# Optimization experiments

Measured on AMD Instinct MI355X. Metric: run time of the kernel, lower is better.

The kernel has to match this reference:

```python
import jax, jax.numpy as jnp
import numpy as np

IN_DIM = 512
CMP_DIM = 512
OUT_DIM = 512
BOARD = (8, 8, 8, 8)
BATCH = 4


def setup_inputs() -> dict:
    key = jax.random.key(0)
    ks = jax.random.split(key, 9)
    shape = (BATCH,) + BOARD + (IN_DIM,)
    query_X = jax.random.normal(ks[0], shape, dtype=jnp.float32)
    key_X = jax.random.normal(ks[1], shape, dtype=jnp.float32)
    value_X = jax.random.normal(ks[2], shape, dtype=jnp.float32)
    s = 1.0 / np.sqrt(IN_DIM)
    W_Q = jax.random.uniform(ks[3], (IN_DIM, CMP_DIM), jnp.float32, -s, s)
    b_Q = jax.random.uniform(ks[4], (CMP_DIM,), jnp.float32, -s, s)
    W_K = jax.random.uniform(ks[5], (IN_DIM, CMP_DIM), jnp.float32, -s, s)
    b_K = jax.random.uniform(ks[6], (CMP_DIM,), jnp.float32, -s, s)
    W_V = jax.random.uniform(ks[7], (IN_DIM, OUT_DIM), jnp.float32, -s, s)
    b_V = jax.random.uniform(ks[8], (OUT_DIM,), jnp.float32, -s, s)
    return {"query_X": query_X, "key_X": key_X, "value_X": value_X,
            "W_Q": W_Q, "b_Q": b_Q, "W_K": W_K, "b_K": b_K, "W_V": W_V, "b_V": b_V}


def reference(query_X, key_X, value_X, W_Q, b_Q, W_K, b_K, W_V, b_V):
    B = query_X.shape[0]
    # project then flatten board dims: (B, N, d)
    q = (query_X @ W_Q + b_Q).reshape(B, -1, CMP_DIM)
    k = (key_X @ W_K + b_K).reshape(B, -1, CMP_DIM)
    v = (value_X @ W_V + b_V).reshape(B, -1, OUT_DIM)
    scores = jnp.einsum('bqc,bkc->bqk', q, k) / jnp.sqrt(jnp.float32(CMP_DIM))
    att = jax.nn.softmax(scores, axis=-1)
    return jnp.einsum('bqk,bkd->bqd', att, v)
```

## Files before the change

### kernel.cpp

```cpp
#include <hip/hip_runtime.h>
#include <hip/hip_bf16.h>
#include <stdint.h>


typedef __attribute__((ext_vector_type(8))) short short8;
typedef __attribute__((ext_vector_type(4))) short short4v;
typedef __attribute__((ext_vector_type(4))) float f32x4;

#define SCALE_L2E 0.06375880243f
#define FIXED_M   12.0f

__device__ __forceinline__ short f2bf(float f) {
    union { float f; uint32_t u; } v; v.f = f;
    uint32_t r = (v.u + 0x7fffu + ((v.u >> 16) & 1u)) >> 16;
    return (short)r;
}

__device__ __forceinline__ f32x4 mfma16x16x32(short8 a, short8 b, f32x4 c) {
    return __builtin_amdgcn_mfma_f32_16x16x32_bf16(a, b, c, 0, 0, 0);
}

#define GLOAD_LDS16(gp, lp)                                                      \
    __builtin_amdgcn_global_load_lds(                                            \
        (const __attribute__((address_space(1))) uint32_t*)(gp),                 \
        (__attribute__((address_space(3))) uint32_t*)(lp), 16, 0, 0)

__global__ __launch_bounds__(256) void cvt_all(
        const float* __restrict__ qX, const float* __restrict__ kX,
        const float* __restrict__ vX,
        const float* __restrict__ WQ, const float* __restrict__ WK,
        const float* __restrict__ WV,
        short* __restrict__ xq, short* __restrict__ xk, short* __restrict__ xv,
        short* __restrict__ wqt, short* __restrict__ wkt, short* __restrict__ wvt) {
    __shared__ float tile[32][33];
    const int y = blockIdx.y;
    if (y < 3) {
        const float* x = y == 0 ? qX : (y == 1 ? kX : vX);
        short*       o = y == 0 ? xq : (y == 1 ? xk : xv);
        int i = blockIdx.x * 256 + threadIdx.x;
        float4 v = ((const float4*)x)[i];
        short4v s;
        s.x = f2bf(v.x); s.y = f2bf(v.y); s.z = f2bf(v.z); s.w = f2bf(v.w);
        ((short4v*)o)[i] = s;
    } else {
        if (blockIdx.x >= 768) return;
        int wz = blockIdx.x >> 8;
        int rem = blockIdx.x & 255;
        int bx = rem & 15, by = rem >> 4;
        const float* src = wz == 0 ? WQ : (wz == 1 ? WK : WV);
        short*       dst = wz == 0 ? wqt : (wz == 1 ? wkt : wvt);
        int tx = threadIdx.x & 31, ty = threadIdx.x >> 5;
        int n0 = bx * 32, k0 = by * 32;
#pragma unroll
        for (int j = 0; j < 32; j += 8)
            tile[ty + j][tx] = src[(size_t)(k0 + ty + j) * 512 + n0 + tx];
        __syncthreads();
#pragma unroll
        for (int j = 0; j < 32; j += 8)
            dst[(size_t)(n0 + ty + j) * 512 + k0 + tx] = f2bf(tile[tx][ty + j]);
    }
}

__device__ __forceinline__ void proj_body(
        const short* __restrict__ Xb, const short* __restrict__ WT,
        const float* __restrict__ bias, short* __restrict__ out, int transpose_v,
        short* sA, short* sB, short* sT) {
    const int tid = threadIdx.x;
    const int w = tid >> 6, lane = tid & 63;
    const int l15 = lane & 15, quad = lane >> 4;
    const int wr = w >> 1, wc = w & 1;
    const int m0 = blockIdx.x * 128;
    const int n0 = blockIdx.y * 128;

    f32x4 acc[4][4];
#pragma unroll
    for (int i = 0; i < 4; ++i)
#pragma unroll
        for (int j = 0; j < 4; ++j) acc[i][j] = f32x4{0.f, 0.f, 0.f, 0.f};

    for (int k0 = 0; k0 < 512; k0 += 64) {
        __syncthreads();
#pragma unroll
        for (int p = 0; p < 4; ++p) {
            int i = p * 256 + tid;
            int row = i >> 3, cl = i & 7, cg = cl ^ (row & 7);
            GLOAD_LDS16(Xb + (size_t)(m0 + row) * 512 + k0 + cg * 8,
                        sA + (size_t)(i & ~63) * 8);
        }
#pragma unroll
        for (int p = 0; p < 4; ++p) {
            int i = p * 256 + tid;
            int row = i >> 3, cl = i & 7, cg = cl ^ (row & 7);
            GLOAD_LDS16(WT + (size_t)(n0 + row) * 512 + k0 + cg * 8,
                        sB + (size_t)(i & ~63) * 8);
        }
        __syncthreads();
#pragma unroll
        for (int ks = 0; ks < 2; ++ks) {
            short8 af[4], bfr[4];
#pragma unroll
            for (int mt = 0; mt < 4; ++mt) {
                int row = wr * 64 + mt * 16 + l15;
                int c = (ks * 4 + quad) ^ (row & 7);
                af[mt] = *(const short8*)&sA[(row * 8 + c) * 8];
            }
#pragma unroll
            for (int nt = 0; nt < 4; ++nt) {
                int row = wc * 64 + nt * 16 + l15;
                int c = (ks * 4 + quad) ^ (row & 7);
                bfr[nt] = *(const short8*)&sB[(row * 8 + c) * 8];
            }
#pragma unroll
            for (int mt = 0; mt < 4; ++mt)
#pragma unroll
                for (int nt = 0; nt < 4; ++nt)
                    acc[mt][nt] = mfma16x16x32(af[mt], bfr[nt], acc[mt][nt]);
        }
    }
    if (!transpose_v) {
#pragma unroll
        for (int nt = 0; nt < 4; ++nt) {
            float bv = bias[n0 + wc * 64 + nt * 16 + l15];
#pragma unroll
            for (int mt = 0; mt < 4; ++mt)
#pragma unroll
                for (int r = 0; r < 4; ++r) {
                    int gm = m0 + wr * 64 + mt * 16 + quad * 4 + r;
                    int gn = n0 + wc * 64 + nt * 16 + l15;
                    out[(size_t)gm * 512 + gn] = f2bf(acc[mt][nt][r] + bv);
                }
        }
    } else {
        __syncthreads();
#pragma unroll
        for (int nt = 0; nt < 4; ++nt) {
            float bv = bias[n0 + wc * 64 + nt * 16 + l15];
            int dl = wc * 64 + nt * 16 + l15;
#pragma unroll
            for (int mt = 0; mt < 4; ++mt) {
                int pl = wr * 64 + mt * 16 + quad * 4;
                short4v s;
                s.x = f2bf(acc[mt][nt][0] + bv);
                s.y = f2bf(acc[mt][nt][1] + bv);
                s.z = f2bf(acc[mt][nt][2] + bv);
                s.w = f2bf(acc[mt][nt][3] + bv);
                *(short4v*)&sT[dl * 136 + pl] = s;
            }
        }
        __syncthreads();
        const int b = m0 >> 12, posb = m0 & 4095;
        const int col = (tid & 15) * 8;
#pragma unroll
        for (int rnd = 0; rnd < 8; ++rnd) {
            int dl = rnd * 16 + (tid >> 4);
            *(short8*)&out[((size_t)b * 512 + n0 + dl) * 4096 + posb + col] =
                *(const short8*)&sT[dl * 136 + col];
        }
    }
}

__global__ __launch_bounds__(256) void proj3(
        const short* __restrict__ xq, const short* __restrict__ xk,
        const short* __restrict__ xv,
        const short* __restrict__ wqt, const short* __restrict__ wkt,
        const short* __restrict__ wvt,
        const float* __restrict__ bQ, const float* __restrict__ bK,
        const float* __restrict__ bV,
        short* __restrict__ oq, short* __restrict__ ok, short* __restrict__ ovt) {
    __shared__ __align__(16) short smem[128 * 136];
    const int z = blockIdx.z;
    proj_body(z == 0 ? xq : (z == 1 ? xk : xv),
              z == 0 ? wqt : (z == 1 ? wkt : wvt),
              z == 0 ? bQ : (z == 1 ? bK : bV),
              z == 0 ? oq : (z == 1 ? ok : ovt), z == 2 ? 1 : 0,
              smem, smem + 8192, smem);
}

__global__ __launch_bounds__(256) void prep_wt(
        const float* __restrict__ wq, const float* __restrict__ wk,
        const float* __restrict__ wv,
        short* __restrict__ wqt, short* __restrict__ wkt, short* __restrict__ wvt) {
    __shared__ float tile[32][33];
    const float* src = blockIdx.z == 0 ? wq : (blockIdx.z == 1 ? wk : wv);
    short*       dst = blockIdx.z == 0 ? wqt : (blockIdx.z == 1 ? wkt : wvt);
    int tx = threadIdx.x, ty = threadIdx.y;
    int n0 = blockIdx.x * 32, k0 = blockIdx.y * 32;
#pragma unroll
    for (int j = 0; j < 32; j += 8)
        tile[ty + j][tx] = src[(size_t)(k0 + ty + j) * 512 + n0 + tx];
    __syncthreads();
#pragma unroll
    for (int j = 0; j < 32; j += 8)
        dst[(size_t)(n0 + ty + j) * 512 + k0 + tx] = f2bf(tile[tx][ty + j]);
}

__global__ __launch_bounds__(256) void x2bf(
        const float* __restrict__ x, short* __restrict__ y) {
    int i = blockIdx.x * 256 + threadIdx.x;
    float4 v = ((const float4*)x)[i];
    short4v s;
    s.x = f2bf(v.x); s.y = f2bf(v.y); s.z = f2bf(v.z); s.w = f2bf(v.w);
    ((short4v*)y)[i] = s;
}

__global__ __launch_bounds__(256) void proj_gemm2(
        const short* __restrict__ Xb, const short* __restrict__ WT,
        const float* __restrict__ bias, short* __restrict__ out, int transpose_v) {
    __shared__ __align__(16) short smem[128 * 136];
    proj_body(Xb, WT, bias, out, transpose_v, smem, smem + 8192, smem);
}

__global__ __launch_bounds__(512, 2) void flash_attn(
        const short* __restrict__ qb, const short* __restrict__ kb,
        const short* __restrict__ vtb, float* __restrict__ out) {
    __shared__ __align__(16) short sK[64 * 64 * 8];
    __shared__ __align__(16) short sV[512 * 8 * 8];
    __shared__ __align__(16) short sP[64 * 72];
    __shared__ __align__(16) float sL[64 * 4];

    const int tid = threadIdx.x;
    const int w = tid >> 6, lane = tid & 63;
    const int l15 = lane & 15, quad = lane >> 4;
    const int qg = w >> 2, kg = w & 3;

    const int n = blockIdx.x + (blockIdx.y << 6);
    const int batch = (n >> 1) & 3;
    const int q0 = ((((n >> 3) << 1) | (n & 1))) << 6;

    const short* qbase = qb  + (size_t)batch * 4096 * 512;
    const short* kbase = kb  + (size_t)batch * 4096 * 512;
    const short* vbase = vtb + (size_t)batch * 512 * 4096;

    const int key0 = tid >> 6;
    const int kcg  = (tid & 63) ^ (key0 & 7);
    const short* ksrc0 = kbase + (size_t)key0 * 512 + kcg * 8;
    const int kdst0 = (tid & ~63) * 8;
    const int d0  = tid >> 3;
    const int vcg = (tid & 7) ^ (d0 & 7);
    const short* vsrc0 = vbase + (size_t)d0 * 4096 + vcg * 8;
    const int vdst0 = (tid & ~63) * 8;

    short8 qf[2][16];
#pragma unroll
    for (int qmt = 0; qmt < 2; ++qmt) {
        const short* qrow = qbase + (size_t)(q0 + qg * 32 + qmt * 16 + l15) * 512 + quad * 8;
#pragma unroll
        for (int ks = 0; ks < 16; ++ks)
            qf[qmt][ks] = *(const short8*)(qrow + ks * 32);
    }

    f32x4 acc[4][4];
#pragma unroll
    for (int i = 0; i < 4; ++i)
#pragma unroll
        for (int j = 0; j < 4; ++j) acc[i][j] = f32x4{0.f, 0.f, 0.f, 0.f};
    float lp[2][4] = {{0.f, 0.f, 0.f, 0.f}, {0.f, 0.f, 0.f, 0.f}};

#pragma unroll
    for (int it = 0; it < 8; ++it)
        GLOAD_LDS16(ksrc0 + it * 4096, sK + kdst0 + it * 4096);
    __syncthreads();

    for (int t = 0; t < 64; ++t) {
        const int t0 = t * 64;

        {
            const short* vp = vsrc0 + t0;
#pragma unroll
            for (int it = 0; it < 8; ++it)
                GLOAD_LDS16(vp + (size_t)it * 262144, sV + vdst0 + it * 4096);
        }
        __builtin_amdgcn_sched_barrier(0);

        f32x4 s0 = f32x4{0.f, 0.f, 0.f, 0.f};
        f32x4 s1 = f32x4{0.f, 0.f, 0.f, 0.f};
        const int key = kg * 16 + l15;
        const int ksw = key & 7;
        __builtin_amdgcn_s_setprio(1);
#pragma unroll
        for (int ks = 0; ks < 16; ++ks) {
            short8 kf = *(const short8*)&sK[(key * 64 + ((ks * 4 + quad) ^ ksw)) * 8];
            s0 = mfma16x16x32(qf[0][ks], kf, s0);
            s1 = mfma16x16x32(qf[1][ks], kf, s1);
        }
        __builtin_amdgcn_s_setprio(0);
#pragma unroll
        for (int qmt = 0; qmt < 2; ++qmt) {
            f32x4 sv = qmt ? s1 : s0;
#pragma unroll
            for (int r = 0; r < 4; ++r) {
                float p = __builtin_amdgcn_exp2f(
                    __builtin_fmaf(sv[r], SCALE_L2E, -FIXED_M));
                lp[qmt][r] += p;
                sP[(qg * 32 + qmt * 16 + quad * 4 + r) * 72 + kg * 16 + l15] = f2bf(p);
            }
        }

        __syncthreads();

        if (t < 63) {
            const short* kp = ksrc0 + (size_t)(t0 + 64) * 512;
#pragma unroll
            for (int it = 0; it < 8; ++it)
                GLOAD_LDS16(kp + it * 4096, sK + kdst0 + it * 4096);
        }
        __builtin_amdgcn_sched_barrier(0);

        __builtin_amdgcn_s_setprio(1);
#pragma unroll
        for (int kc = 0; kc < 2; ++kc) {
            short8 pa[4], vf[4];
#pragma unroll
            for (int mt = 0; mt < 4; ++mt)
                pa[mt] = *(const short8*)&sP[(mt * 16 + l15) * 72 + kc * 32 + quad * 8];
#pragma unroll
            for (int nt = 0; nt < 4; ++nt) {
                int d = w * 64 + nt * 16 + l15;
                vf[nt] = *(const short8*)&sV[(d * 8 + ((kc * 4 + quad) ^ (d & 7))) * 8];
            }
#pragma unroll
            for (int mt = 0; mt < 4; ++mt)
#pragma unroll
                for (int nt = 0; nt < 4; ++nt)
                    acc[mt][nt] = mfma16x16x32(pa[mt], vf[nt], acc[mt][nt]);
        }
        __builtin_amdgcn_s_setprio(0);

        __syncthreads();
    }
#pragma unroll
    for (int qmt = 0; qmt < 2; ++qmt)
#pragma unroll
        for (int r = 0; r < 4; ++r) {
            float v = lp[qmt][r];
            v += __shfl_xor(v, 1);
            v += __shfl_xor(v, 2);
            v += __shfl_xor(v, 4);
            v += __shfl_xor(v, 8);
            if (l15 == 0)
                sL[(qg * 32 + qmt * 16 + quad * 4 + r) * 4 + kg] = v;
        }
    __syncthreads();
#pragma unroll
    for (int mt = 0; mt < 4; ++mt)
#pragma unroll
        for (int r = 0; r < 4; ++r) {
            int row = mt * 16 + quad * 4 + r;
            float linv = 1.0f / (sL[row * 4] + sL[row * 4 + 1] +
                                 sL[row * 4 + 2] + sL[row * 4 + 3]);
            float* orow = out + ((size_t)batch * 4096 + q0 + row) * 512 + w * 64 + l15;
#pragma unroll
            for (int nt = 0; nt < 4; ++nt)
                orow[nt * 16] = acc[mt][nt][r] * linv;
        }
}

extern "C" void kernel_launch(void* const* d_in, const int* in_sizes, int n_in,
                              void* d_out, int out_size, void* d_ws, size_t ws_size,
                              hipStream_t stream) {
    const float* qX = (const float*)d_in[0];
    const float* kX = (const float*)d_in[1];
    const float* vX = (const float*)d_in[2];
    const float* WQ = (const float*)d_in[3];
    const float* bQ = (const float*)d_in[4];
    const float* WK = (const float*)d_in[5];
    const float* bK = (const float*)d_in[6];
    const float* WV = (const float*)d_in[7];
    const float* bV = (const float*)d_in[8];
    float* out = (float*)d_out;

    short* qb  = (short*)d_ws;
    short* kb  = qb  + (size_t)16384 * 512;
    short* vtb = kb  + (size_t)16384 * 512;
    short* wqt = vtb + (size_t)16384 * 512;
    short* wkt = wqt + (size_t)512 * 512;
    short* wvt = wkt + (size_t)512 * 512;
    short* xq  = wvt + (size_t)512 * 512;

    if (ws_size >= (size_t)102236160) {
        short* xk = xq + (size_t)16384 * 512;
        short* xv = xk + (size_t)16384 * 512;
        cvt_all<<<dim3(8192, 4), 256, 0, stream>>>(qX, kX, vX, WQ, WK, WV,
                                                   xq, xk, xv, wqt, wkt, wvt);
        proj3<<<dim3(128, 4, 3), 256, 0, stream>>>(xq, xk, xv, wqt, wkt, wvt,
                                                   bQ, bK, bV, qb, kb, vtb);
    } else {
        prep_wt<<<dim3(16, 16, 3), dim3(32, 8), 0, stream>>>(WQ, WK, WV, wqt, wkt, wvt);
        x2bf<<<8192, 256, 0, stream>>>(qX, xq);
        proj_gemm2<<<dim3(128, 4), 256, 0, stream>>>(xq, wqt, bQ, qb, 0);
        x2bf<<<8192, 256, 0, stream>>>(kX, xq);
        proj_gemm2<<<dim3(128, 4), 256, 0, stream>>>(xq, wkt, bK, kb, 0);
        x2bf<<<8192, 256, 0, stream>>>(vX, xq);
        proj_gemm2<<<dim3(128, 4), 256, 0, stream>>>(xq, wvt, bV, vtb, 1);
    }
    flash_attn<<<dim3(64, 4), 512, 0, stream>>>(qb, kb, vtb, out);
}
```

Before: 359.1 us.

## Shrink flash-attention tiles to 32 queries x 32 keys with 256-thread blocks

Restructures the attention kernel from 64-query blocks of 512 threads with 64-key steps to 32-query blocks of 256 threads with 32-key steps, doubling the grid to 512 blocks. Each wave now owns 128 output columns and one 16-row score tile, and the K/V LDS layouts and swizzles are reworked to match. The s_setprio hints are removed. The aim is more blocks in flight across the CUs with a smaller LDS footprint, in exchange for reading K and V twice as often in total and running twice as many loop iterations and barriers.

```diff
diff --git a/kernel.cpp b/kernel.cpp
--- a/kernel.cpp
+++ b/kernel.cpp
@@ -210,147 +210,133 @@
     proj_body(Xb, WT, bias, out, transpose_v, smem, smem + 8192, smem);
 }
 
-__global__ __launch_bounds__(512, 2) void flash_attn(
+__global__ __launch_bounds__(256, 2) void flash_attn(
         const short* __restrict__ qb, const short* __restrict__ kb,
         const short* __restrict__ vtb, float* __restrict__ out) {
-    __shared__ __align__(16) short sK[64 * 64 * 8];
-    __shared__ __align__(16) short sV[512 * 8 * 8];
-    __shared__ __align__(16) short sP[64 * 72];
-    __shared__ __align__(16) float sL[64 * 4];
+    __shared__ __align__(16) short sK[32 * 512];
+    __shared__ __align__(16) short sV[512 * 32];
+    __shared__ __align__(16) short sP[32 * 56];
+    __shared__ __align__(16) float sL[32 * 2];
 
     const int tid = threadIdx.x;
     const int w = tid >> 6, lane = tid & 63;
     const int l15 = lane & 15, quad = lane >> 4;
-    const int qg = w >> 2, kg = w & 3;
-
-    const int n = blockIdx.x + (blockIdx.y << 6);
+    const int qg = w >> 1, kg = w & 1;
+
+    const int n = blockIdx.x + (blockIdx.y << 7);
     const int batch = (n >> 1) & 3;
-    const int q0 = ((((n >> 3) << 1) | (n & 1))) << 6;
+    const int q0 = ((((n >> 3) << 1) | (n & 1))) << 5;
 
     const short* qbase = qb  + (size_t)batch * 4096 * 512;
     const short* kbase = kb  + (size_t)batch * 4096 * 512;
     const short* vbase = vtb + (size_t)batch * 512 * 4096;
 
-    const int key0 = tid >> 6;
-    const int kcg  = (tid & 63) ^ (key0 & 7);
-    const short* ksrc0 = kbase + (size_t)key0 * 512 + kcg * 8;
+    const int ko0 = (lane ^ (w & 7)) * 8;
+    const int ko1 = (lane ^ ((w + 4) & 7)) * 8;
     const int kdst0 = (tid & ~63) * 8;
-    const int d0  = tid >> 3;
-    const int vcg = (tid & 7) ^ (d0 & 7);
-    const short* vsrc0 = vbase + (size_t)d0 * 4096 + vcg * 8;
+
+    const short* vsrc0 = vbase + (size_t)(tid >> 2) * 4096
+                       + (((tid & 3) ^ ((tid >> 3) & 3)) * 8);
     const int vdst0 = (tid & ~63) * 8;
 
-    short8 qf[2][16];
-#pragma unroll
-    for (int qmt = 0; qmt < 2; ++qmt) {
-        const short* qrow = qbase + (size_t)(q0 + qg * 32 + qmt * 16 + l15) * 512 + quad * 8;
+    short8 qf[16];
+    {
+        const short* qrow = qbase + (size_t)(q0 + qg * 16 + l15) * 512 + quad * 8;
 #pragma unroll
         for (int ks = 0; ks < 16; ++ks)
-            qf[qmt][ks] = *(const short8*)(qrow + ks * 32);
-    }
-
-    f32x4 acc[4][4];
-#pragma unroll
-    for (int i = 0; i < 4; ++i)
-#pragma unroll
-        for (int j = 0; j < 4; ++j) acc[i][j] = f32x4{0.f, 0.f, 0.f, 0.f};
-    float lp[2][4] = {{0.f, 0.f, 0.f, 0.f}, {0.f, 0.f, 0.f, 0.f}};
+            qf[ks] = *(const short8*)(qrow + ks * 32);
+    }
+
+    f32x4 acc[2][8];
+#pragma unroll
+    for (int i = 0; i < 2; ++i)
+#pragma unroll
+        for (int j = 0; j < 8; ++j) acc[i][j] = f32x4{0.f, 0.f, 0.f, 0.f};
+    float lp[4] = {0.f, 0.f, 0.f, 0.f};
 
 #pragma unroll
     for (int it = 0; it < 8; ++it)
-        GLOAD_LDS16(ksrc0 + it * 4096, sK + kdst0 + it * 4096);
+        GLOAD_LDS16(kbase + (size_t)(it * 4 + w) * 512 + ((it & 1) ? ko1 : ko0),
+                    sK + it * 2048 + kdst0);
     __syncthreads();
 
-    for (int t = 0; t < 64; ++t) {
-        const int t0 = t * 64;
+    for (int t = 0; t < 128; ++t) {
+        const int t0 = t * 32;
 
         {
             const short* vp = vsrc0 + t0;
 #pragma unroll
             for (int it = 0; it < 8; ++it)
-                GLOAD_LDS16(vp + (size_t)it * 262144, sV + vdst0 + it * 4096);
+                GLOAD_LDS16(vp + (size_t)it * 262144, sV + it * 2048 + vdst0);
         }
         __builtin_amdgcn_sched_barrier(0);
 
         f32x4 s0 = f32x4{0.f, 0.f, 0.f, 0.f};
-        f32x4 s1 = f32x4{0.f, 0.f, 0.f, 0.f};
         const int key = kg * 16 + l15;
         const int ksw = key & 7;
-        __builtin_amdgcn_s_setprio(1);
 #pragma unroll
         for (int ks = 0; ks < 16; ++ks) {
             short8 kf = *(const short8*)&sK[(key * 64 + ((ks * 4 + quad) ^ ksw)) * 8];
-            s0 = mfma16x16x32(qf[0][ks], kf, s0);
-            s1 = mfma16x16x32(qf[1][ks], kf, s1);
-        }
-        __builtin_amdgcn_s_setprio(0);
-#pragma unroll
-        for (int qmt = 0; qmt < 2; ++qmt) {
-            f32x4 sv = qmt ? s1 : s0;
-#pragma unroll
-            for (int r = 0; r < 4; ++r) {
-                float p = __builtin_amdgcn_exp2f(
-                    __builtin_fmaf(sv[r], SCALE_L2E, -FIXED_M));
-                lp[qmt][r] += p;
-                sP[(qg * 32 + qmt * 16 + quad * 4 + r) * 72 + kg * 16 + l15] = f2bf(p);
+            s0 = mfma16x16x32(qf[ks], kf, s0);
+        }
+#pragma unroll
+        for (int r = 0; r < 4; ++r) {
+            float p = __builtin_amdgcn_exp2f(
+                __builtin_fmaf(s0[r], SCALE_L2E, -FIXED_M));
+            lp[r] += p;
+            sP[(qg * 16 + quad * 4 + r) * 56 + kg * 16 + l15] = f2bf(p);
+        }
+
+        __syncthreads();
+
+        if (t < 127) {
+            const short* kp = kbase + (size_t)(t0 + 32 + w) * 512;
+#pragma unroll
+            for (int it = 0; it < 8; ++it)
+                GLOAD_LDS16(kp + (size_t)it * 2048 + ((it & 1) ? ko1 : ko0),
+                            sK + it * 2048 + kdst0);
+        }
+        __builtin_amdgcn_sched_barrier(0);
+
+        {
+            short8 pa[2], vf[8];
+#pragma unroll
+            for (int mt = 0; mt < 2; ++mt)
+                pa[mt] = *(const short8*)&sP[(mt * 16 + l15) * 56 + quad * 8];
+#pragma unroll
+            for (int nt = 0; nt < 8; ++nt) {
+                int d = w * 128 + nt * 16 + l15;
+                vf[nt] = *(const short8*)&sV[d * 32 + ((quad ^ ((d >> 1) & 3)) * 8)];
             }
-        }
-
-        __syncthreads();
-
-        if (t < 63) {
-            const short* kp = ksrc0 + (size_t)(t0 + 64) * 512;
-#pragma unroll
-            for (int it = 0; it < 8; ++it)
-                GLOAD_LDS16(kp + it * 4096, sK + kdst0 + it * 4096);
-        }
-        __builtin_amdgcn_sched_barrier(0);
-
-        __builtin_amdgcn_s_setprio(1);
-#pragma unroll
-        for (int kc = 0; kc < 2; ++kc) {
-            short8 pa[4], vf[4];
-#pragma unroll
-            for (int mt = 0; mt < 4; ++mt)
-                pa[mt] = *(const short8*)&sP[(mt * 16 + l15) * 72 + kc * 32 + quad * 8];
-#pragma unroll
-            for (int nt = 0; nt < 4; ++nt) {
-                int d = w * 64 + nt * 16 + l15;
-                vf[nt] = *(const short8*)&sV[(d * 8 + ((kc * 4 + quad) ^ (d & 7))) * 8];
-            }
-#pragma unroll
-            for (int mt = 0; mt < 4; ++mt)
-#pragma unroll
-                for (int nt = 0; nt < 4; ++nt)
+#pragma unroll
+            for (int mt = 0; mt < 2; ++mt)
+#pragma unroll
+                for (int nt = 0; nt < 8; ++nt)
                     acc[mt][nt] = mfma16x16x32(pa[mt], vf[nt], acc[mt][nt]);
         }
-        __builtin_amdgcn_s_setprio(0);
-
-        __syncthreads();
-    }
-#pragma unroll
-    for (int qmt = 0; qmt < 2; ++qmt)
-#pragma unroll
-        for (int r = 0; r < 4; ++r) {
-            float v = lp[qmt][r];
-            v += __shfl_xor(v, 1);
-            v += __shfl_xor(v, 2);
-            v += __shfl_xor(v, 4);
-            v += __shfl_xor(v, 8);
-            if (l15 == 0)
-                sL[(qg * 32 + qmt * 16 + quad * 4 + r) * 4 + kg] = v;
-        }
+
+        __syncthreads();
+    }
+#pragma unroll
+    for (int r = 0; r < 4; ++r) {
+        float v = lp[r];
+        v += __shfl_xor(v, 1);
+        v += __shfl_xor(v, 2);
+        v += __shfl_xor(v, 4);
+        v += __shfl_xor(v, 8);
+        if (l15 == 0)
+            sL[(qg * 16 + quad * 4 + r) * 2 + kg] = v;
+    }
     __syncthreads();
 #pragma unroll
-    for (int mt = 0; mt < 4; ++mt)
+    for (int mt = 0; mt < 2; ++mt)
 #pragma unroll
         for (int r = 0; r < 4; ++r) {
             int row = mt * 16 + quad * 4 + r;
-            float linv = 1.0f / (sL[row * 4] + sL[row * 4 + 1] +
-                                 sL[row * 4 + 2] + sL[row * 4 + 3]);
-            float* orow = out + ((size_t)batch * 4096 + q0 + row) * 512 + w * 64 + l15;
-#pragma unroll
-            for (int nt = 0; nt < 4; ++nt)
+            float linv = 1.0f / (sL[row * 2] + sL[row * 2 + 1]);
+            float* orow = out + ((size_t)batch * 4096 + q0 + row) * 512 + w * 128 + l15;
+#pragma unroll
+            for (int nt = 0; nt < 8; ++nt)
                 orow[nt * 16] = acc[mt][nt][r] * linv;
         }
 }
@@ -393,5 +379,5 @@
         x2bf<<<8192, 256, 0, stream>>>(vX, xq);
         proj_gemm2<<<dim3(128, 4), 256, 0, stream>>>(xq, wvt, bV, vtb, 1);
     }
-    flash_attn<<<dim3(64, 4), 512, 0, stream>>>(qb, kb, vtb, out);
-}
+    flash_attn<<<dim3(128, 4), 256, 0, stream>>>(qb, kb, vtb, out);
+}
```

Result: slower. 397.5 us (+10.7%).

## Fuse fp32-to-bf16 activation conversion into projection GEMM loads

Applied to the files above, without the earlier changes.

Removes the separate activation conversion pass and its bf16 workspace. The projection GEMM now reads fp32 activations directly into registers, packs them with v_cvt_pk_bf16_f32, and writes the swizzled tile to LDS, while weights still go through direct global-to-LDS loads. This saves a full write and reread of three 32 MB bf16 activation copies, at the cost of GEMM tiles reading twice the bytes through registers instead of async LDS loads, and the ws-size branch goes away. It also drops the s_setprio hints in the attention kernel.

```diff
diff --git a/kernel.cpp b/kernel.cpp
--- a/kernel.cpp
+++ b/kernel.cpp
@@ -24,157 +24,6 @@
     __builtin_amdgcn_global_load_lds(                                            \
         (const __attribute__((address_space(1))) uint32_t*)(gp),                 \
         (__attribute__((address_space(3))) uint32_t*)(lp), 16, 0, 0)
-
-__global__ __launch_bounds__(256) void cvt_all(
-        const float* __restrict__ qX, const float* __restrict__ kX,
-        const float* __restrict__ vX,
-        const float* __restrict__ WQ, const float* __restrict__ WK,
-        const float* __restrict__ WV,
-        short* __restrict__ xq, short* __restrict__ xk, short* __restrict__ xv,
-        short* __restrict__ wqt, short* __restrict__ wkt, short* __restrict__ wvt) {
-    __shared__ float tile[32][33];
-    const int y = blockIdx.y;
-    if (y < 3) {
-        const float* x = y == 0 ? qX : (y == 1 ? kX : vX);
-        short*       o = y == 0 ? xq : (y == 1 ? xk : xv);
-        int i = blockIdx.x * 256 + threadIdx.x;
-        float4 v = ((const float4*)x)[i];
-        short4v s;
-        s.x = f2bf(v.x); s.y = f2bf(v.y); s.z = f2bf(v.z); s.w = f2bf(v.w);
-        ((short4v*)o)[i] = s;
-    } else {
-        if (blockIdx.x >= 768) return;
-        int wz = blockIdx.x >> 8;
-        int rem = blockIdx.x & 255;
-        int bx = rem & 15, by = rem >> 4;
-        const float* src = wz == 0 ? WQ : (wz == 1 ? WK : WV);
-        short*       dst = wz == 0 ? wqt : (wz == 1 ? wkt : wvt);
-        int tx = threadIdx.x & 31, ty = threadIdx.x >> 5;
-        int n0 = bx * 32, k0 = by * 32;
-#pragma unroll
-        for (int j = 0; j < 32; j += 8)
-            tile[ty + j][tx] = src[(size_t)(k0 + ty + j) * 512 + n0 + tx];
-        __syncthreads();
-#pragma unroll
-        for (int j = 0; j < 32; j += 8)
-            dst[(size_t)(n0 + ty + j) * 512 + k0 + tx] = f2bf(tile[tx][ty + j]);
-    }
-}
-
-__device__ __forceinline__ void proj_body(
-        const short* __restrict__ Xb, const short* __restrict__ WT,
-        const float* __restrict__ bias, short* __restrict__ out, int transpose_v,
-        short* sA, short* sB, short* sT) {
-    const int tid = threadIdx.x;
-    const int w = tid >> 6, lane = tid & 63;
-    const int l15 = lane & 15, quad = lane >> 4;
-    const int wr = w >> 1, wc = w & 1;
-    const int m0 = blockIdx.x * 128;
-    const int n0 = blockIdx.y * 128;
-
-    f32x4 acc[4][4];
-#pragma unroll
-    for (int i = 0; i < 4; ++i)
-#pragma unroll
-        for (int j = 0; j < 4; ++j) acc[i][j] = f32x4{0.f, 0.f, 0.f, 0.f};
-
-    for (int k0 = 0; k0 < 512; k0 += 64) {
-        __syncthreads();
-#pragma unroll
-        for (int p = 0; p < 4; ++p) {
-            int i = p * 256 + tid;
-            int row = i >> 3, cl = i & 7, cg = cl ^ (row & 7);
-            GLOAD_LDS16(Xb + (size_t)(m0 + row) * 512 + k0 + cg * 8,
-                        sA + (size_t)(i & ~63) * 8);
-        }
-#pragma unroll
-        for (int p = 0; p < 4; ++p) {
-            int i = p * 256 + tid;
-            int row = i >> 3, cl = i & 7, cg = cl ^ (row & 7);
-            GLOAD_LDS16(WT + (size_t)(n0 + row) * 512 + k0 + cg * 8,
-                        sB + (size_t)(i & ~63) * 8);
-        }
-        __syncthreads();
-#pragma unroll
-        for (int ks = 0; ks < 2; ++ks) {
-            short8 af[4], bfr[4];
-#pragma unroll
-            for (int mt = 0; mt < 4; ++mt) {
-                int row = wr * 64 + mt * 16 + l15;
-                int c = (ks * 4 + quad) ^ (row & 7);
-                af[mt] = *(const short8*)&sA[(row * 8 + c) * 8];
-            }
-#pragma unroll
-            for (int nt = 0; nt < 4; ++nt) {
-                int row = wc * 64 + nt * 16 + l15;
-                int c = (ks * 4 + quad) ^ (row & 7);
-                bfr[nt] = *(const short8*)&sB[(row * 8 + c) * 8];
-            }
-#pragma unroll
-            for (int mt = 0; mt < 4; ++mt)
-#pragma unroll
-                for (int nt = 0; nt < 4; ++nt)
-                    acc[mt][nt] = mfma16x16x32(af[mt], bfr[nt], acc[mt][nt]);
-        }
-    }
-    if (!transpose_v) {
-#pragma unroll
-        for (int nt = 0; nt < 4; ++nt) {
-            float bv = bias[n0 + wc * 64 + nt * 16 + l15];
-#pragma unroll
-            for (int mt = 0; mt < 4; ++mt)
-#pragma unroll
-                for (int r = 0; r < 4; ++r) {
-                    int gm = m0 + wr * 64 + mt * 16 + quad * 4 + r;
-                    int gn = n0 + wc * 64 + nt * 16 + l15;
-                    out[(size_t)gm * 512 + gn] = f2bf(acc[mt][nt][r] + bv);
-                }
-        }
-    } else {
-        __syncthreads();
-#pragma unroll
-        for (int nt = 0; nt < 4; ++nt) {
-            float bv = bias[n0 + wc * 64 + nt * 16 + l15];
-            int dl = wc * 64 + nt * 16 + l15;
-#pragma unroll
-            for (int mt = 0; mt < 4; ++mt) {
-                int pl = wr * 64 + mt * 16 + quad * 4;
-                short4v s;
-                s.x = f2bf(acc[mt][nt][0] + bv);
-                s.y = f2bf(acc[mt][nt][1] + bv);
-                s.z = f2bf(acc[mt][nt][2] + bv);
-                s.w = f2bf(acc[mt][nt][3] + bv);
-                *(short4v*)&sT[dl * 136 + pl] = s;
-            }
-        }
-        __syncthreads();
-        const int b = m0 >> 12, posb = m0 & 4095;
-        const int col = (tid & 15) * 8;
-#pragma unroll
-        for (int rnd = 0; rnd < 8; ++rnd) {
-            int dl = rnd * 16 + (tid >> 4);
-            *(short8*)&out[((size_t)b * 512 + n0 + dl) * 4096 + posb + col] =
-                *(const short8*)&sT[dl * 136 + col];
-        }
-    }
-}
-
-__global__ __launch_bounds__(256) void proj3(
-        const short* __restrict__ xq, const short* __restrict__ xk,
-        const short* __restrict__ xv,
-        const short* __restrict__ wqt, const short* __restrict__ wkt,
-        const short* __restrict__ wvt,
-        const float* __restrict__ bQ, const float* __restrict__ bK,
-        const float* __restrict__ bV,
-        short* __restrict__ oq, short* __restrict__ ok, short* __restrict__ ovt) {
-    __shared__ __align__(16) short smem[128 * 136];
-    const int z = blockIdx.z;
-    proj_body(z == 0 ? xq : (z == 1 ? xk : xv),
-              z == 0 ? wqt : (z == 1 ? wkt : wvt),
-              z == 0 ? bQ : (z == 1 ? bK : bV),
-              z == 0 ? oq : (z == 1 ? ok : ovt), z == 2 ? 1 : 0,
-              smem, smem + 8192, smem);
-}
 
 __global__ __launch_bounds__(256) void prep_wt(
         const float* __restrict__ wq, const float* __restrict__ wk,
@@ -194,20 +43,135 @@
         dst[(size_t)(n0 + ty + j) * 512 + k0 + tx] = f2bf(tile[tx][ty + j]);
 }
 
-__global__ __launch_bounds__(256) void x2bf(
-        const float* __restrict__ x, short* __restrict__ y) {
-    int i = blockIdx.x * 256 + threadIdx.x;
-    float4 v = ((const float4*)x)[i];
-    short4v s;
-    s.x = f2bf(v.x); s.y = f2bf(v.y); s.z = f2bf(v.z); s.w = f2bf(v.w);
-    ((short4v*)y)[i] = s;
-}
-
-__global__ __launch_bounds__(256) void proj_gemm2(
-        const short* __restrict__ Xb, const short* __restrict__ WT,
-        const float* __restrict__ bias, short* __restrict__ out, int transpose_v) {
+__device__ __forceinline__ void proj_body(
+        const float* __restrict__ Xf, const short* __restrict__ WT,
+        const float* __restrict__ bias, short* __restrict__ out, int transpose_v,
+        short* sA, short* sB, short* sT) {
+    const int tid = threadIdx.x;
+    const int w = tid >> 6, lane = tid & 63;
+    const int l15 = lane & 15, quad = lane >> 4;
+    const int wr = w >> 1, wc = w & 1;
+    const int m0 = blockIdx.x * 128;
+    const int n0 = blockIdx.y * 128;
+
+    f32x4 acc[4][4];
+#pragma unroll
+    for (int i = 0; i < 4; ++i)
+#pragma unroll
+        for (int j = 0; j < 4; ++j) acc[i][j] = f32x4{0.f, 0.f, 0.f, 0.f};
+
+    for (int k0 = 0; k0 < 512; k0 += 64) {
+        __syncthreads();
+        float4 av[4][2];
+#pragma unroll
+        for (int p = 0; p < 4; ++p) {
+            int i = p * 256 + tid;
+            int row = i >> 3, cl = i & 7;
+            const float4* src = (const float4*)(Xf + (size_t)(m0 + row) * 512 + k0 + cl * 8);
+            av[p][0] = src[0];
+            av[p][1] = src[1];
+        }
+#pragma unroll
+        for (int p = 0; p < 4; ++p) {
+            int i = p * 256 + tid;
+            int row = i >> 3, cl = i & 7, cg = cl ^ (row & 7);
+            GLOAD_LDS16(WT + (size_t)(n0 + row) * 512 + k0 + cg * 8,
+                        sB + (size_t)(i & ~63) * 8);
+        }
+#pragma unroll
+        for (int p = 0; p < 4; ++p) {
+            int i = p * 256 + tid;
+            int row = i >> 3, cl = i & 7, cg = cl ^ (row & 7);
+            uint32_t u0, u1, u2, u3;
+            asm("v_cvt_pk_bf16_f32 %0, %1, %2" : "=v"(u0) : "v"(av[p][0].x), "v"(av[p][0].y));
+            asm("v_cvt_pk_bf16_f32 %0, %1, %2" : "=v"(u1) : "v"(av[p][0].z), "v"(av[p][0].w));
+            asm("v_cvt_pk_bf16_f32 %0, %1, %2" : "=v"(u2) : "v"(av[p][1].x), "v"(av[p][1].y));
+            asm("v_cvt_pk_bf16_f32 %0, %1, %2" : "=v"(u3) : "v"(av[p][1].z), "v"(av[p][1].w));
+            short8 s;
+            ((uint32_t*)&s)[0] = u0; ((uint32_t*)&s)[1] = u1;
+            ((uint32_t*)&s)[2] = u2; ((uint32_t*)&s)[3] = u3;
+            *(short8*)&sA[(size_t)(row * 8 + cg) * 8] = s;
+        }
+        __syncthreads();
+#pragma unroll
+        for (int ks = 0; ks < 2; ++ks) {
+            short8 af[4], bfr[4];
+#pragma unroll
+            for (int mt = 0; mt < 4; ++mt) {
+                int row = wr * 64 + mt * 16 + l15;
+                int c = (ks * 4 + quad) ^ (row & 7);
+                af[mt] = *(const short8*)&sA[(row * 8 + c) * 8];
+            }
+#pragma unroll
+            for (int nt = 0; nt < 4; ++nt) {
+                int row = wc * 64 + nt * 16 + l15;
+                int c = (ks * 4 + quad) ^ (row & 7);
+                bfr[nt] = *(const short8*)&sB[(row * 8 + c) * 8];
+            }
+#pragma unroll
+            for (int mt = 0; mt < 4; ++mt)
+#pragma unroll
+                for (int nt = 0; nt < 4; ++nt)
+                    acc[mt][nt] = mfma16x16x32(af[mt], bfr[nt], acc[mt][nt]);
+        }
+    }
+    if (!transpose_v) {
+#pragma unroll
+        for (int nt = 0; nt < 4; ++nt) {
+            float bv = bias[n0 + wc * 64 + nt * 16 + l15];
+#pragma unroll
+            for (int mt = 0; mt < 4; ++mt)
+#pragma unroll
+                for (int r = 0; r < 4; ++r) {
+                    int gm = m0 + wr * 64 + mt * 16 + quad * 4 + r;
+                    int gn = n0 + wc * 64 + nt * 16 + l15;
+                    out[(size_t)gm * 512 + gn] = f2bf(acc[mt][nt][r] + bv);
+                }
+        }
+    } else {
+        __syncthreads();
+#pragma unroll
+        for (int nt = 0; nt < 4; ++nt) {
+            float bv = bias[n0 + wc * 64 + nt * 16 + l15];
+            int dl = wc * 64 + nt * 16 + l15;
+#pragma unroll
+            for (int mt = 0; mt < 4; ++mt) {
+                int pl = wr * 64 + mt * 16 + quad * 4;
+                short4v s;
+                s.x = f2bf(acc[mt][nt][0] + bv);
+                s.y = f2bf(acc[mt][nt][1] + bv);
+                s.z = f2bf(acc[mt][nt][2] + bv);
+                s.w = f2bf(acc[mt][nt][3] + bv);
+                *(short4v*)&sT[dl * 136 + pl] = s;
+            }
+        }
+        __syncthreads();
+        const int b = m0 >> 12, posb = m0 & 4095;
+        const int col = (tid & 15) * 8;
+#pragma unroll
+        for (int rnd = 0; rnd < 8; ++rnd) {
+            int dl = rnd * 16 + (tid >> 4);
+            *(short8*)&out[((size_t)b * 512 + n0 + dl) * 4096 + posb + col] =
+                *(const short8*)&sT[dl * 136 + col];
+        }
+    }
+}
+
+__global__ __launch_bounds__(256) void proj3(
+        const float* __restrict__ qX, const float* __restrict__ kX,
+        const float* __restrict__ vX,
+        const short* __restrict__ wqt, const short* __restrict__ wkt,
+        const short* __restrict__ wvt,
+        const float* __restrict__ bQ, const float* __restrict__ bK,
+        const float* __restrict__ bV,
+        short* __restrict__ oq, short* __restrict__ ok, short* __restrict__ ovt) {
     __shared__ __align__(16) short smem[128 * 136];
-    proj_body(Xb, WT, bias, out, transpose_v, smem, smem + 8192, smem);
+    const int z = blockIdx.z;
+    proj_body(z == 0 ? qX : (z == 1 ? kX : vX),
+              z == 0 ? wqt : (z == 1 ? wkt : wvt),
+              z == 0 ? bQ : (z == 1 ? bK : bV),
+              z == 0 ? oq : (z == 1 ? ok : ovt), z == 2 ? 1 : 0,
+              smem, smem + 8192, smem);
 }
 
 __global__ __launch_bounds__(512, 2) void flash_attn(
@@ -276,14 +240,12 @@
         f32x4 s1 = f32x4{0.f, 0.f, 0.f, 0.f};
         const int key = kg * 16 + l15;
         const int ksw = key & 7;
-        __builtin_amdgcn_s_setprio(1);
 #pragma unroll
         for (int ks = 0; ks < 16; ++ks) {
             short8 kf = *(const short8*)&sK[(key * 64 + ((ks * 4 + quad) ^ ksw)) * 8];
             s0 = mfma16x16x32(qf[0][ks], kf, s0);
             s1 = mfma16x16x32(qf[1][ks], kf, s1);
         }
-        __builtin_amdgcn_s_setprio(0);
 #pragma unroll
         for (int qmt = 0; qmt < 2; ++qmt) {
             f32x4 sv = qmt ? s1 : s0;
@@ -306,7 +268,6 @@
         }
         __builtin_amdgcn_sched_barrier(0);
 
-        __builtin_amdgcn_s_setprio(1);
 #pragma unroll
         for (int kc = 0; kc < 2; ++kc) {
             short8 pa[4], vf[4];
@@ -324,7 +285,6 @@
                 for (int nt = 0; nt < 4; ++nt)
                     acc[mt][nt] = mfma16x16x32(pa[mt], vf[nt], acc[mt][nt]);
         }
-        __builtin_amdgcn_s_setprio(0);
 
         __syncthreads();
     }
@@ -375,23 +335,9 @@
     short* wqt = vtb + (size_t)16384 * 512;
     short* wkt = wqt + (size_t)512 * 512;
     short* wvt = wkt + (size_t)512 * 512;
-    short* xq  = wvt + (size_t)512 * 512;
-
-    if (ws_size >= (size_t)102236160) {
-        short* xk = xq + (size_t)16384 * 512;
-        short* xv = xk + (size_t)16384 * 512;
-        cvt_all<<<dim3(8192, 4), 256, 0, stream>>>(qX, kX, vX, WQ, WK, WV,
-                                                   xq, xk, xv, wqt, wkt, wvt);
-        proj3<<<dim3(128, 4, 3), 256, 0, stream>>>(xq, xk, xv, wqt, wkt, wvt,
-                                                   bQ, bK, bV, qb, kb, vtb);
-    } else {
-        prep_wt<<<dim3(16, 16, 3), dim3(32, 8), 0, stream>>>(WQ, WK, WV, wqt, wkt, wvt);
-        x2bf<<<8192, 256, 0, stream>>>(qX, xq);
-        proj_gemm2<<<dim3(128, 4), 256, 0, stream>>>(xq, wqt, bQ, qb, 0);
-        x2bf<<<8192, 256, 0, stream>>>(kX, xq);
-        proj_gemm2<<<dim3(128, 4), 256, 0, stream>>>(xq, wkt, bK, kb, 0);
-        x2bf<<<8192, 256, 0, stream>>>(vX, xq);
-        proj_gemm2<<<dim3(128, 4), 256, 0, stream>>>(xq, wvt, bV, vtb, 1);
-    }
+
+    prep_wt<<<dim3(16, 16, 3), dim3(32, 8), 0, stream>>>(WQ, WK, WV, wqt, wkt, wvt);
+    proj3<<<dim3(128, 4, 3), 256, 0, stream>>>(qX, kX, vX, wqt, wkt, wvt,
+                                               bQ, bK, bV, qb, kb, vtb);
     flash_attn<<<dim3(64, 4), 512, 0, stream>>>(qb, kb, vtb, out);
 }
```

Measured after the change: 340.7 us. -5.1%, faster.
